# Performance work log

Measured on AMD Instinct MI355X. Metric: run time of the kernel, lower is better.

## Reference

```python
import jax, jax.numpy as jnp
import numpy as np
from functools import partial

WIN = 11  # SSIM window
PAD = WIN // 2
C1 = 0.01 ** 2
C2 = 0.03 ** 2
W_SAMPLED, W_PERC, W_STRUCT, W_TEMP = 0.3, 0.4, 0.2, 0.1


def _avg_pool(x):
    # torch F.avg_pool2d(window=11, stride=1, pad=5, count_include_pad=True)
    s = jax.lax.reduce_window(x, 0.0, jax.lax.add,
                              window_dimensions=(1, 1, WIN, WIN),
                              window_strides=(1, 1, 1, 1),
                              padding=[(0, 0), (0, 0), (PAD, PAD), (PAD, PAD)])
    return s / (WIN * WIN)


def _ssim(x, y):
    mu_x = _avg_pool(x)
    mu_y = _avg_pool(y)
    sigma_x = _avg_pool(x * x) - mu_x ** 2
    sigma_y = _avg_pool(y * y) - mu_y ** 2
    sigma_xy = _avg_pool(x * y) - mu_x * mu_y
    ssim = (2 * mu_x * mu_y + C1) * (2 * sigma_xy + C2) / ((mu_x ** 2 + mu_y ** 2 + C1) * (sigma_x + sigma_y + C2))
    return ssim.mean()


def setup_inputs() -> dict:
    key = jax.random.key(0)
    k1, k2, k3, k4 = jax.random.split(key, 4)
    B, C, H, W = 16, 3, 512, 512
    N = 4096
    prediction = jax.random.normal(k1, (B, C, H, W), dtype=jnp.float32)
    target = jax.random.normal(k2, (B, C, H, W), dtype=jnp.float32)
    sampled_positions = jax.random.randint(k3, (N, 2), 0, H, dtype=jnp.int64)
    importance_map = jax.random.uniform(k4, (B, 1, H, W), dtype=jnp.float32)
    return {"prediction": prediction, "target": target,
            "sampled_positions": sampled_positions, "importance_map": importance_map}


def reference(prediction, target, sampled_positions, importance_map):
    N = sampled_positions.shape[0]
    u = sampled_positions[:, 0]  # index into H
    v = sampled_positions[:, 1]  # index into W
    # gather sampled pixels: [B, C, N]
    pred_px = prediction[:, :, u, v]
    targ_px = target[:, :, u, v]
    # per-position MSE over (B, C)
    mse_n = jnp.mean((pred_px - targ_px) ** 2, axis=(0, 1))  # [N]
    # per-position weight: mean over (B, 1) of 1/(importance + 0.1)
    w_n = jnp.mean(1.0 / (importance_map[:, :, u, v] + 0.1), axis=(0, 1))  # [N]
    sampled_loss = jnp.sum(w_n * mse_n) / max(N, 1)

    perceptual_loss = jnp.mean(jnp.abs(prediction - target))
    structural_loss = 1.0 - _ssim(prediction, target)
    temporal_loss = jnp.array(0.0, dtype=prediction.dtype)  # prev_pred is None on first call

    total = (W_SAMPLED * sampled_loss + W_PERC * perceptual_loss +
             W_STRUCT * structural_loss + W_TEMP * temporal_loss)
    return (total, sampled_loss, perceptual_loss, structural_loss, temporal_loss)
```

## Files before the change

kernel.cpp:

```cpp
#include <hip/hip_runtime.h>

#define IMG_H 512
#define IMG_W 512
#define IMGSZ (IMG_H * IMG_W)
#define NIMG 48
#define NB 16
#define NPOS 4096
#define DNPIX 12582912.0

#define RB 8
#define WPB 4
#define BLOCK_ROWS (RB * WPB)
#define BGRPS (IMG_H / BLOCK_ROWS)
#define SSIM_BLOCKS (NIMG * BGRPS)
#define TOTAL_BLOCKS SSIM_BLOCKS

__device__ __forceinline__ void load8(const float* __restrict__ base, float x[8])
{
    const float4* p = (const float4*)base;
    float4 a = p[0], b = p[1];
    x[0] = a.x; x[1] = a.y; x[2] = a.z; x[3] = a.w;
    x[4] = b.x; x[5] = b.y; x[6] = b.z; x[7] = b.w;
}

__device__ __forceinline__ float horiz_ssim4(const float V[4][8], int lane)
{
    float W[4][8];
#pragma unroll
    for (int q = 0; q < 4; ++q) {
        float A0 = V[q][0];
        float A1 = A0 + V[q][1];
        float A2 = A1 + V[q][2];
        float A3 = A2 + V[q][3];
        float A4 = A3 + V[q][4];
        float A5 = A4 + V[q][5];
        float A6 = A5 + V[q][6];
        float T  = A6 + V[q][7];
        float B1 = T - A0, B2 = T - A1, B3 = T - A2, B4 = T - A3;
        float B5 = T - A4, B6 = T - A5, B7 = T - A6;
        float LB3 = __shfl_up(B3, 1), LB4 = __shfl_up(B4, 1);
        float LB5 = __shfl_up(B5, 1), LB6 = __shfl_up(B6, 1);
        float LB7 = __shfl_up(B7, 1);
        float RA0 = __shfl_down(A0, 1), RA1 = __shfl_down(A1, 1);
        float RA2 = __shfl_down(A2, 1), RA3 = __shfl_down(A3, 1);
        float RA4 = __shfl_down(A4, 1);
        if (lane == 0)  { LB3 = LB4 = LB5 = LB6 = LB7 = 0.f; }
        if (lane == 63) { RA0 = RA1 = RA2 = RA3 = RA4 = 0.f; }
        W[q][0] = LB3 + A5;
        W[q][1] = LB4 + A6;
        W[q][2] = LB5 + T;
        W[q][3] = LB6 + T + RA0;
        W[q][4] = LB7 + T + RA1;
        W[q][5] = T + RA2;
        W[q][6] = B1 + RA3;
        W[q][7] = B2 + RA4;
    }
    const float inv121 = 1.0f / 121.0f;
    const float inv121x2 = 2.0f / 121.0f;
    const float C1c = 1e-4f, CC = 1e-4f + 9e-4f;
    float s = 0.f;
#pragma unroll
    for (int j = 0; j < 8; ++j) {
        float mux = W[0][j] * inv121;
        float muy = W[1][j] * inv121;
        float den1 = fmaf(mux, mux, fmaf(muy, muy, C1c));
        float num1 = fmaf(mux + mux, muy, C1c);
        float den2 = fmaf(W[2][j], inv121, CC - den1);
        float num2 = fmaf(W[3][j], inv121x2, CC - num1);
        s += __fdividef(num1 * num2, den1 * den2);
    }
    return s;
}

__global__ __launch_bounds__(256) void fused_kernel(
    const float* __restrict__ pred, const float* __restrict__ targ,
    const int* __restrict__ pos32, const float* __restrict__ imp,
    double* __restrict__ acc, unsigned int* __restrict__ cnt,
    float* __restrict__ out)
{
    const int tid = threadIdx.x;
    const int lane = tid & 63;
    const int wid = tid >> 6;
    const int bid = blockIdx.x;
    float ssim_s = 0.f, perc = 0.f, samp = 0.f;

    int s = (bid & 7) * (SSIM_BLOCKS / 8) + (bid >> 3);
    const int img = s >> 4;
    const int bg = s & 15;
    const int rs = bg * BLOCK_ROWS + wid * RB;
    const float* __restrict__ pimg = pred + (size_t)img * IMGSZ;
    const float* __restrict__ timg = targ + (size_t)img * IMGSZ;
    const int c0 = lane * 8;

    float V[4][8];
#pragma unroll
    for (int q = 0; q < 4; ++q)
#pragma unroll
        for (int k = 0; k < 8; ++k) V[q][k] = 0.f;

    float cx[8], cy[8];
    float cm;
    {
        int gr = rs - 5;
        int gc = max(gr, 0);
        cm = (gr == gc) ? 1.f : 0.f;
        load8(pimg + (size_t)gc * IMG_W + c0, cx);
        load8(timg + (size_t)gc * IMG_W + c0, cy);
    }
    for (int kk = 0; kk < 11; ++kk) {
        float m = cm;
        bool pin = (kk >= 5);
        float xs[8], ys[8];
#pragma unroll
        for (int k = 0; k < 8; ++k) { xs[k] = cx[k] * m; ys[k] = cy[k] * m; }
        int gr2 = rs - 4 + kk;
        int gc2 = min(max(gr2, 0), IMG_H - 1);
        cm = (gr2 == gc2) ? 1.f : 0.f;
        load8(pimg + (size_t)gc2 * IMG_W + c0, cx);
        load8(timg + (size_t)gc2 * IMG_W + c0, cy);
#pragma unroll
        for (int k = 0; k < 8; ++k) {
            V[0][k] += xs[k];
            V[1][k] += ys[k];
            V[2][k] = fmaf(xs[k], xs[k], fmaf(ys[k], ys[k], V[2][k]));
            V[3][k] = fmaf(xs[k], ys[k], V[3][k]);
            perc += pin ? fabsf(xs[k] - ys[k]) : 0.f;
        }
    }
    float lx[8], ly[8];
    float lm;
    {
        int gl = rs - 5;
        int glc = max(gl, 0);
        lm = (gl == glc) ? 1.f : 0.f;
        load8(pimg + (size_t)glc * IMG_W + c0, lx);
        load8(timg + (size_t)glc * IMG_W + c0, ly);
    }
    ssim_s += horiz_ssim4(V, lane);

    for (int r = 1; r < RB; ++r) {
        float cme = cm, cml = lm;
        bool pin = (r < 3);
        float ae[8], be[8], al[8], bl[8];
#pragma unroll
        for (int k = 0; k < 8; ++k) {
            ae[k] = cx[k] * cme; be[k] = cy[k] * cme;
            al[k] = lx[k] * cml; bl[k] = ly[k] * cml;
        }
        int ge2 = rs + r + 6;
        int gl2 = rs + r - 5;
        int gec = min(ge2, IMG_H - 1);
        int glc = max(gl2, 0);
        cm = (ge2 == gec) ? 1.f : 0.f;
        lm = (gl2 == glc) ? 1.f : 0.f;
        load8(pimg + (size_t)gec * IMG_W + c0, cx);
        load8(timg + (size_t)gec * IMG_W + c0, cy);
        load8(pimg + (size_t)glc * IMG_W + c0, lx);
        load8(timg + (size_t)glc * IMG_W + c0, ly);
#pragma unroll
        for (int k = 0; k < 8; ++k) {
            V[0][k] += ae[k] - al[k];
            V[1][k] += be[k] - bl[k];
            V[2][k] += fmaf(ae[k], ae[k], fmaf(be[k], be[k],
                       -fmaf(al[k], al[k], bl[k] * bl[k])));
            V[3][k] += fmaf(ae[k], be[k], -al[k] * bl[k]);
            perc += pin ? fabsf(ae[k] - be[k]) : 0.f;
        }
        ssim_s += horiz_ssim4(V, lane);
    }

    {
        int n0 = (bid * NPOS) / SSIM_BLOCKS;
        int n1 = ((bid + 1) * NPOS) / SSIM_BLOCKS;
        unsigned long long ball = __ballot(pos32[2 * lane + 1] != 0);
        for (int n = n0 + wid; n < n1; n += WPB) {
            int u, v;
            if (ball == 0ull) { u = pos32[4 * n]; v = pos32[4 * n + 2]; }
            else              { u = pos32[2 * n]; v = pos32[2 * n + 1]; }
            int off = u * IMG_W + v;
            float a = 0.f, w = 0.f;
            if (lane < NIMG) {
                float d = pred[(size_t)lane * IMGSZ + off]
                        - targ[(size_t)lane * IMGSZ + off];
                a = d * d;
            } else {
                w = 1.0f / (imp[(size_t)(lane - NIMG) * IMGSZ + off] + 0.1f);
            }
#pragma unroll
            for (int o = 32; o > 0; o >>= 1) {
                a += __shfl_down(a, o);
                w += __shfl_down(w, o);
            }
            if (lane == 0)
                samp += (w * (1.0f / 16.0f)) * (a * (1.0f / 48.0f));
        }
    }

#pragma unroll
    for (int o = 32; o > 0; o >>= 1) {
        ssim_s += __shfl_down(ssim_s, o);
        perc   += __shfl_down(perc, o);
    }
    __shared__ float red[3][WPB];
    if (lane == 0) { red[0][wid] = ssim_s; red[1][wid] = perc; red[2][wid] = samp; }
    __syncthreads();
    if (tid == 0) {
        float ss = 0.f, pp = 0.f, mm = 0.f;
#pragma unroll
        for (int k = 0; k < WPB; ++k) {
            ss += red[0][k]; pp += red[1][k]; mm += red[2][k];
        }
        atomicAdd(&acc[0], (double)ss);
        atomicAdd(&acc[1], (double)pp);
        atomicAdd(&acc[2], (double)mm);
        __threadfence();
        unsigned int old = atomicAdd(cnt, 1u);
        if (old == TOTAL_BLOCKS - 1) {
            double s0 = atomicAdd(&acc[0], 0.0);
            double s1 = atomicAdd(&acc[1], 0.0);
            double s2 = atomicAdd(&acc[2], 0.0);
            double sampled = s2 / (double)NPOS;
            double perceptual = s1 / DNPIX;
            double structural = 1.0 - s0 / DNPIX;
            double total = 0.3 * sampled + 0.4 * perceptual + 0.2 * structural;
            out[0] = (float)total;
            out[1] = (float)sampled;
            out[2] = (float)perceptual;
            out[3] = (float)structural;
            out[4] = 0.0f;
        }
    }
}

extern "C" void kernel_launch(void* const* d_in, const int* in_sizes, int n_in,
                              void* d_out, int out_size, void* d_ws, size_t ws_size,
                              hipStream_t stream)
{
    const float* pred = (const float*)d_in[0];
    const float* targ = (const float*)d_in[1];
    const int* pos = (const int*)d_in[2];
    const float* imp = (const float*)d_in[3];
    float* out = (float*)d_out;
    double* acc = (double*)d_ws;
    unsigned int* cnt = (unsigned int*)((char*)d_ws + 24);

    hipMemsetAsync(d_ws, 0, 32, stream);
    hipLaunchKernelGGL(fused_kernel, dim3(TOTAL_BLOCKS), dim3(256), 0, stream,
                       pred, targ, pos, imp, acc, cnt, out);
}
```

Before: 92.18 us.

## Split each image row across two waves with shared-memory seam exchange

```diff
diff --git a/kernel.cpp b/kernel.cpp
--- a/kernel.cpp
+++ b/kernel.cpp
@@ -4,72 +4,21 @@
 #define IMG_W 512
 #define IMGSZ (IMG_H * IMG_W)
 #define NIMG 48
-#define NB 16
 #define NPOS 4096
 #define DNPIX 12582912.0
 
 #define RB 8
 #define WPB 4
-#define BLOCK_ROWS (RB * WPB)
+#define BLOCK_ROWS 16
 #define BGRPS (IMG_H / BLOCK_ROWS)
 #define SSIM_BLOCKS (NIMG * BGRPS)
 #define TOTAL_BLOCKS SSIM_BLOCKS
-
-__device__ __forceinline__ void load8(const float* __restrict__ base, float x[8])
+#define HALF_W 256
+
+__device__ __forceinline__ void load4(const float* __restrict__ base, float x[4])
 {
-    const float4* p = (const float4*)base;
-    float4 a = p[0], b = p[1];
+    float4 a = *(const float4*)base;
     x[0] = a.x; x[1] = a.y; x[2] = a.z; x[3] = a.w;
-    x[4] = b.x; x[5] = b.y; x[6] = b.z; x[7] = b.w;
-}
-
-__device__ __forceinline__ float horiz_ssim4(const float V[4][8], int lane)
-{
-    float W[4][8];
-#pragma unroll
-    for (int q = 0; q < 4; ++q) {
-        float A0 = V[q][0];
-        float A1 = A0 + V[q][1];
-        float A2 = A1 + V[q][2];
-        float A3 = A2 + V[q][3];
-        float A4 = A3 + V[q][4];
-        float A5 = A4 + V[q][5];
-        float A6 = A5 + V[q][6];
-        float T  = A6 + V[q][7];
-        float B1 = T - A0, B2 = T - A1, B3 = T - A2, B4 = T - A3;
-        float B5 = T - A4, B6 = T - A5, B7 = T - A6;
-        float LB3 = __shfl_up(B3, 1), LB4 = __shfl_up(B4, 1);
-        float LB5 = __shfl_up(B5, 1), LB6 = __shfl_up(B6, 1);
-        float LB7 = __shfl_up(B7, 1);
-        float RA0 = __shfl_down(A0, 1), RA1 = __shfl_down(A1, 1);
-        float RA2 = __shfl_down(A2, 1), RA3 = __shfl_down(A3, 1);
-        float RA4 = __shfl_down(A4, 1);
-        if (lane == 0)  { LB3 = LB4 = LB5 = LB6 = LB7 = 0.f; }
-        if (lane == 63) { RA0 = RA1 = RA2 = RA3 = RA4 = 0.f; }
-        W[q][0] = LB3 + A5;
-        W[q][1] = LB4 + A6;
-        W[q][2] = LB5 + T;
-        W[q][3] = LB6 + T + RA0;
-        W[q][4] = LB7 + T + RA1;
-        W[q][5] = T + RA2;
-        W[q][6] = B1 + RA3;
-        W[q][7] = B2 + RA4;
-    }
-    const float inv121 = 1.0f / 121.0f;
-    const float inv121x2 = 2.0f / 121.0f;
-    const float C1c = 1e-4f, CC = 1e-4f + 9e-4f;
-    float s = 0.f;
-#pragma unroll
-    for (int j = 0; j < 8; ++j) {
-        float mux = W[0][j] * inv121;
-        float muy = W[1][j] * inv121;
-        float den1 = fmaf(mux, mux, fmaf(muy, muy, C1c));
-        float num1 = fmaf(mux + mux, muy, C1c);
-        float den2 = fmaf(W[2][j], inv121, CC - den1);
-        float num2 = fmaf(W[3][j], inv121x2, CC - num1);
-        s += __fdividef(num1 * num2, den1 * den2);
-    }
-    return s;
 }
 
 __global__ __launch_bounds__(256) void fused_kernel(
@@ -78,48 +27,139 @@
     double* __restrict__ acc, unsigned int* __restrict__ cnt,
     float* __restrict__ out)
 {
+    __shared__ float seamS[2][2][4][5];
+    __shared__ float seamP[2][2][4][5];
+    __shared__ float red[3][WPB];
+
     const int tid = threadIdx.x;
     const int lane = tid & 63;
     const int wid = tid >> 6;
+    const int half = wid & 1;
+    const int brow = wid >> 1;
     const int bid = blockIdx.x;
     float ssim_s = 0.f, perc = 0.f, samp = 0.f;
 
     int s = (bid & 7) * (SSIM_BLOCKS / 8) + (bid >> 3);
-    const int img = s >> 4;
-    const int bg = s & 15;
-    const int rs = bg * BLOCK_ROWS + wid * RB;
+    const int img = s >> 5;
+    const int bg = s & 31;
+    const int rs = bg * BLOCK_ROWS + brow * RB;
     const float* __restrict__ pimg = pred + (size_t)img * IMGSZ;
     const float* __restrict__ timg = targ + (size_t)img * IMGSZ;
-    const int c0 = lane * 8;
-
-    float V[4][8];
+    const int c0 = half * HALF_W + lane * 4;
+
+    const float inv121 = 1.0f / 121.0f;
+    const float inv121x2 = 2.0f / 121.0f;
+    const float C1c = 1e-4f, CC = 1e-4f + 9e-4f;
+
+    float V[4][4];
 #pragma unroll
     for (int q = 0; q < 4; ++q)
 #pragma unroll
-        for (int k = 0; k < 8; ++k) V[q][k] = 0.f;
-
-    float cx[8], cy[8];
+        for (int k = 0; k < 4; ++k) V[q][k] = 0.f;
+
+#define HORIZ(PAR)                                                            \
+    {                                                                         \
+        float A1[4], A2[4], T[4], B1[4], B2[4], B3[4];                        \
+        _Pragma("unroll")                                                     \
+        for (int q = 0; q < 4; ++q) {                                         \
+            A1[q] = V[q][0] + V[q][1];                                        \
+            A2[q] = A1[q] + V[q][2];                                          \
+            T[q]  = A2[q] + V[q][3];                                          \
+            B1[q] = T[q] - V[q][0];                                           \
+            B2[q] = T[q] - A1[q];                                             \
+            B3[q] = T[q] - A2[q];                                             \
+        }                                                                     \
+        _Pragma("unroll")                                                     \
+        for (int q = 0; q < 4; ++q) {                                         \
+            float ls1 = __shfl_up(B3[q], 1);       \
+            float na0 = __shfl_down(V[q][0], 1);   \
+            if (half == 0 && lane == 63) {                                    \
+                seamS[PAR][brow][q][0] = B3[q];                   \
+                seamS[PAR][brow][q][1] = B2[q];                   \
+                seamS[PAR][brow][q][2] = B1[q];                   \
+                seamS[PAR][brow][q][3] = T[q];                    \
+                seamS[PAR][brow][q][4] = T[q] + ls1;              \
+            }                                                                 \
+            if (half == 1 && lane == 0) {                                     \
+                seamP[PAR][brow][q][0] = V[q][0];                \
+                seamP[PAR][brow][q][1] = A1[q];                  \
+                seamP[PAR][brow][q][2] = A2[q];                  \
+                seamP[PAR][brow][q][3] = T[q];                   \
+                seamP[PAR][brow][q][4] = T[q] + na0;             \
+            }                                                                 \
+        }                                                                     \
+        __syncthreads();                                                      \
+        float Wq[4][4];                                                       \
+        _Pragma("unroll")                                                     \
+        for (int q = 0; q < 4; ++q) {                                         \
+            float pT   = __shfl_up(T[q], 1);                                  \
+            float pB1  = __shfl_up(B1[q], 1);                                 \
+            float pB2  = __shfl_up(B2[q], 1);                                 \
+            float ppB3 = __shfl_up(B3[q], 2);                                 \
+            float nA1  = __shfl_down(A1[q], 1);                               \
+            float nA2  = __shfl_down(A2[q], 1);                               \
+            float nT   = __shfl_down(T[q], 1);                                \
+            float nnA0 = __shfl_down(V[q][0], 2);                             \
+            float S1e = 0.f, S2e = 0.f, S3e = 0.f, S4e = 0.f, S5e = 0.f;      \
+            float P1e = 0.f, P2e = 0.f, P3e = 0.f, P4e = 0.f, P5e = 0.f;      \
+            if (half == 1) {                                                  \
+                S1e = seamS[PAR][brow][q][0]; S2e = seamS[PAR][brow][q][1];   \
+                S3e = seamS[PAR][brow][q][2]; S4e = seamS[PAR][brow][q][3];   \
+                S5e = seamS[PAR][brow][q][4];                                 \
+            } else {                                                          \
+                P1e = seamP[PAR][brow][q][0]; P2e = seamP[PAR][brow][q][1];   \
+                P3e = seamP[PAR][brow][q][2]; P4e = seamP[PAR][brow][q][3];   \
+                P5e = seamP[PAR][brow][q][4];                                 \
+            }                                                                 \
+            float left5 = (lane == 0) ? S5e                                   \
+                          : (((lane == 1) ? S1e : ppB3) + pT);                \
+            float left4 = (lane == 0) ? S4e : pT;                             \
+            float left3 = (lane == 0) ? S3e : pB1;                            \
+            float left2 = (lane == 0) ? S2e : pB2;                            \
+            float r0 = (lane == 63) ? P2e : nA1;                              \
+            float r1 = (lane == 63) ? P3e : nA2;                              \
+            float r2 = (lane == 63) ? P4e : nT;                               \
+            float r3 = (lane == 63) ? P5e                                     \
+                       : (nT + ((lane == 62) ? P1e : nnA0));                  \
+            Wq[q][0] = left5 + T[q] + r0;                                     \
+            Wq[q][1] = left4 + T[q] + r1;                                     \
+            Wq[q][2] = left3 + T[q] + r2;                                     \
+            Wq[q][3] = left2 + T[q] + r3;                                     \
+        }                                                                     \
+        _Pragma("unroll")                                                     \
+        for (int j = 0; j < 4; ++j) {                                         \
+            float mux = Wq[0][j] * inv121;                                    \
+            float muy = Wq[1][j] * inv121;                                    \
+            float den1 = fmaf(mux, mux, fmaf(muy, muy, C1c));                 \
+            float num1 = fmaf(mux + mux, muy, C1c);                           \
+            float den2 = fmaf(Wq[2][j], inv121, CC - den1);                   \
+            float num2 = fmaf(Wq[3][j], inv121x2, CC - num1);                 \
+            ssim_s += __fdividef(num1 * num2, den1 * den2);                   \
+        }                                                                     \
+    }
+
+    float cx[4], cy[4];
     float cm;
     {
         int gr = rs - 5;
         int gc = max(gr, 0);
         cm = (gr == gc) ? 1.f : 0.f;
-        load8(pimg + (size_t)gc * IMG_W + c0, cx);
-        load8(timg + (size_t)gc * IMG_W + c0, cy);
+        load4(pimg + (size_t)gc * IMG_W + c0, cx);
+        load4(timg + (size_t)gc * IMG_W + c0, cy);
     }
     for (int kk = 0; kk < 11; ++kk) {
         float m = cm;
         bool pin = (kk >= 5);
-        float xs[8], ys[8];
-#pragma unroll
-        for (int k = 0; k < 8; ++k) { xs[k] = cx[k] * m; ys[k] = cy[k] * m; }
+        float xs[4], ys[4];
+#pragma unroll
+        for (int k = 0; k < 4; ++k) { xs[k] = cx[k] * m; ys[k] = cy[k] * m; }
         int gr2 = rs - 4 + kk;
         int gc2 = min(max(gr2, 0), IMG_H - 1);
         cm = (gr2 == gc2) ? 1.f : 0.f;
-        load8(pimg + (size_t)gc2 * IMG_W + c0, cx);
-        load8(timg + (size_t)gc2 * IMG_W + c0, cy);
-#pragma unroll
-        for (int k = 0; k < 8; ++k) {
+        load4(pimg + (size_t)gc2 * IMG_W + c0, cx);
+        load4(timg + (size_t)gc2 * IMG_W + c0, cy);
+#pragma unroll
+        for (int k = 0; k < 4; ++k) {
             V[0][k] += xs[k];
             V[1][k] += ys[k];
             V[2][k] = fmaf(xs[k], xs[k], fmaf(ys[k], ys[k], V[2][k]));
@@ -127,23 +167,23 @@
             perc += pin ? fabsf(xs[k] - ys[k]) : 0.f;
         }
     }
-    float lx[8], ly[8];
+    float lx[4], ly[4];
     float lm;
     {
         int gl = rs - 5;
         int glc = max(gl, 0);
         lm = (gl == glc) ? 1.f : 0.f;
-        load8(pimg + (size_t)glc * IMG_W + c0, lx);
-        load8(timg + (size_t)glc * IMG_W + c0, ly);
-    }
-    ssim_s += horiz_ssim4(V, lane);
+        load4(pimg + (size_t)glc * IMG_W + c0, lx);
+        load4(timg + (size_t)glc * IMG_W + c0, ly);
+    }
+    HORIZ(0)
 
     for (int r = 1; r < RB; ++r) {
         float cme = cm, cml = lm;
         bool pin = (r < 3);
-        float ae[8], be[8], al[8], bl[8];
-#pragma unroll
-        for (int k = 0; k < 8; ++k) {
+        float ae[4], be[4], al[4], bl[4];
+#pragma unroll
+        for (int k = 0; k < 4; ++k) {
             ae[k] = cx[k] * cme; be[k] = cy[k] * cme;
             al[k] = lx[k] * cml; bl[k] = ly[k] * cml;
         }
@@ -153,12 +193,12 @@
         int glc = max(gl2, 0);
         cm = (ge2 == gec) ? 1.f : 0.f;
         lm = (gl2 == glc) ? 1.f : 0.f;
-        load8(pimg + (size_t)gec * IMG_W + c0, cx);
-        load8(timg + (size_t)gec * IMG_W + c0, cy);
-        load8(pimg + (size_t)glc * IMG_W + c0, lx);
-        load8(timg + (size_t)glc * IMG_W + c0, ly);
-#pragma unroll
-        for (int k = 0; k < 8; ++k) {
+        load4(pimg + (size_t)gec * IMG_W + c0, cx);
+        load4(timg + (size_t)gec * IMG_W + c0, cy);
+        load4(pimg + (size_t)glc * IMG_W + c0, lx);
+        load4(timg + (size_t)glc * IMG_W + c0, ly);
+#pragma unroll
+        for (int k = 0; k < 4; ++k) {
             V[0][k] += ae[k] - al[k];
             V[1][k] += be[k] - bl[k];
             V[2][k] += fmaf(ae[k], ae[k], fmaf(be[k], be[k],
@@ -166,8 +206,9 @@
             V[3][k] += fmaf(ae[k], be[k], -al[k] * bl[k]);
             perc += pin ? fabsf(ae[k] - be[k]) : 0.f;
         }
-        ssim_s += horiz_ssim4(V, lane);
-    }
+        HORIZ(r & 1)
+    }
+#undef HORIZ
 
     {
         int n0 = (bid * NPOS) / SSIM_BLOCKS;
@@ -201,7 +242,6 @@
         ssim_s += __shfl_down(ssim_s, o);
         perc   += __shfl_down(perc, o);
     }
-    __shared__ float red[3][WPB];
     if (lane == 0) { red[0][wid] = ssim_s; red[1][wid] = perc; red[2][wid] = samp; }
     __syncthreads();
     if (tid == 0) {
```

Measured after the change: 148.6 us. +61.2%, slower.
